# Performance work log

Measured on AMD Instinct MI355X. Metric: run time of the kernel, lower is better.

The kernel has to match this reference:

```python
import jax, jax.numpy as jnp
import numpy as np

INPUT_DIM = 1024
HIDDEN_DIM = 1024


def setup_inputs() -> dict:
    key = jax.random.key(0)
    k1, k2, k3, k4, k5 = jax.random.split(key, 5)
    B, T = 64, 512
    bound_h = 1.0 / np.sqrt(HIDDEN_DIM)
    bound_x = 1.0 / np.sqrt(INPUT_DIM)
    return {
        "x_seq": jax.random.normal(k1, (B, T, INPUT_DIM), dtype=jnp.float32),
        "W_h": jax.random.uniform(k2, (HIDDEN_DIM, HIDDEN_DIM), jnp.float32, -bound_h, bound_h),
        "b_h": jax.random.uniform(k3, (HIDDEN_DIM,), jnp.float32, -bound_h, bound_h),
        "W_x": jax.random.uniform(k4, (HIDDEN_DIM, INPUT_DIM), jnp.float32, -bound_x, bound_x),
        "b_x": jax.random.uniform(k5, (HIDDEN_DIM,), jnp.float32, -bound_x, bound_x),
    }


def reference(x_seq, W_h, b_h, W_x, b_x):
    # Precompute input projection for all timesteps as one batched GEMM:
    # xp: [B, T, H]
    xp = jnp.einsum("bti,hi->bth", x_seq, W_x) + b_x
    B = x_seq.shape[0]
    h0 = jnp.zeros((B, HIDDEN_DIM), dtype=x_seq.dtype)

    def step(h, xp_t):
        # h: [B, H], xp_t: [B, H]
        h_new = jnp.tanh(h @ W_h.T + b_h + xp_t)
        return h_new, None

    # scan over time: xp transposed to [T, B, H]
    h_final, _ = jax.lax.scan(step, h0, jnp.swapaxes(xp, 0, 1))
    return h_final  # [B, H] — last hidden state per batch element
```

## Files before the change

kernel.cpp:

```cpp
#include <hip/hip_runtime.h>
#include <cmath>


#define Bsz 64
#define Tsz 512
#define Hsz 1024

typedef float  f32x4 __attribute__((ext_vector_type(4)));
typedef short  s16x8 __attribute__((ext_vector_type(8)));

#define AS1 __attribute__((address_space(1)))
#define AS3 __attribute__((address_space(3)))

__device__ __forceinline__ unsigned short f2bf(float f) {
  unsigned u = __float_as_uint(f);
  u += 0x7fff + ((u >> 16) & 1);
  return (unsigned short)(u >> 16);
}

__device__ __forceinline__ void pack8(unsigned short* d, float4 v0, float4 v1) {
  d[0] = f2bf(v0.x); d[1] = f2bf(v0.y); d[2] = f2bf(v0.z); d[3] = f2bf(v0.w);
  d[4] = f2bf(v1.x); d[5] = f2bf(v1.y); d[6] = f2bf(v1.z); d[7] = f2bf(v1.w);
}

__device__ __forceinline__ float fast_tanh(float x) {
  float e = __expf(2.0f * x);
  return 1.0f - 2.0f / (e + 1.0f);
}

__global__ __launch_bounds__(256) void cvt_kernel(
    const float* __restrict__ x, const float* __restrict__ Wx,
    unsigned short* __restrict__ xb, unsigned short* __restrict__ wxb) {
  const long long NX = (long long)Bsz * Tsz * Hsz / 8;
  const long long NW = (long long)Hsz * Hsz / 8;
  const long long stride = (long long)gridDim.x * 256;
  for (long long i = (long long)blockIdx.x * 256 + threadIdx.x;
       i < NX + NW; i += stride) {
    const float* s; unsigned short* d; long long j;
    if (i < NX) { s = x;  d = xb;  j = i; }
    else        { s = Wx; d = wxb; j = i - NX; }
    const float4 a = *(const float4*)(s + j * 8);
    const float4 b = *(const float4*)(s + j * 8 + 4);
    unsigned short tmp[8];
    pack8(tmp, a, b);
    *(s16x8*)(d + j * 8) = *(const s16x8*)tmp;
  }
}

__global__ __launch_bounds__(256) void xp_gemm128_kernel(
    const unsigned short* __restrict__ xb, const unsigned short* __restrict__ wxb,
    const float* __restrict__ bx, const float* __restrict__ bh,
    float* __restrict__ xp) {
  __shared__ __align__(16) unsigned short Al[128 * 32];
  __shared__ __align__(16) unsigned short Bl[128 * 32];

  const int tid  = threadIdx.x;
  const int w    = tid >> 6;
  const int lane = tid & 63;
  const int m    = lane & 15;
  const int q    = lane >> 4;
  const int wy   = w >> 1;
  const int wx   = w & 1;
  const int row0 = blockIdx.x * 128;
  const int col0 = blockIdx.y * 128;

  f32x4 acc[4][4];
#pragma unroll
  for (int i = 0; i < 4; ++i)
#pragma unroll
    for (int j = 0; j < 4; ++j) acc[i][j] = (f32x4){0.f, 0.f, 0.f, 0.f};

  const int lrow = lane >> 2;
  const int lch  = lane & 3;

  for (int kt = 0; kt < 32; ++kt) {
    const int kb = kt * 32;
#pragma unroll
    for (int i = 0; i < 2; ++i) {
      const int ra  = w * 32 + i * 16 + lrow;
      const int scs = lch ^ ((ra >> 1) & 3);
      const unsigned short* gA = xb  + (size_t)(row0 + ra) * 1024 + kb + scs * 8;
      const unsigned short* gB = wxb + (size_t)(col0 + ra) * 1024 + kb + scs * 8;
      __builtin_amdgcn_global_load_lds(
          (const AS1 void*)gA, (AS3 void*)&Al[(w * 32 + i * 16) * 32], 16, 0, 0);
      __builtin_amdgcn_global_load_lds(
          (const AS1 void*)gB, (AS3 void*)&Bl[(w * 32 + i * 16) * 32], 16, 0, 0);
    }
    __syncthreads();

    s16x8 af[4], bf[4];
#pragma unroll
    for (int mt = 0; mt < 4; ++mt) {
      const int ar = wy * 64 + mt * 16 + m;
      af[mt] = *(const s16x8*)&Al[ar * 32 + ((q ^ ((ar >> 1) & 3)) << 3)];
    }
#pragma unroll
    for (int nt = 0; nt < 4; ++nt) {
      const int br = wx * 64 + nt * 16 + m;
      bf[nt] = *(const s16x8*)&Bl[br * 32 + ((q ^ ((br >> 1) & 3)) << 3)];
    }
#pragma unroll
    for (int mt = 0; mt < 4; ++mt)
#pragma unroll
      for (int nt = 0; nt < 4; ++nt)
        acc[mt][nt] = __builtin_amdgcn_mfma_f32_16x16x32_bf16(
            af[mt], bf[nt], acc[mt][nt], 0, 0, 0);
    __syncthreads();
  }

#pragma unroll
  for (int nt = 0; nt < 4; ++nt) {
    const int col  = col0 + wx * 64 + nt * 16 + m;
    const float bias = bx[col] + bh[col];
#pragma unroll
    for (int mt = 0; mt < 4; ++mt) {
#pragma unroll
      for (int r = 0; r < 4; ++r) {
        const int rowg = row0 + wy * 64 + mt * 16 + q * 4 + r;
        const int b = rowg >> 9;
        const int t = rowg & 511;
        xp[(size_t)t * (Bsz * Hsz) + b * Hsz + col] = acc[mt][nt][r] + bias;
      }
    }
  }
}

__global__ __launch_bounds__(256) void xp_gemm_f32_kernel(
    const float* __restrict__ x, const float* __restrict__ Wx,
    const float* __restrict__ bx, const float* __restrict__ bh,
    float* __restrict__ xp) {
  __shared__ unsigned short Al[64 * 32];
  __shared__ unsigned short Bl[64 * 32];

  const int tid  = threadIdx.x;
  const int w    = tid >> 6;
  const int lane = tid & 63;
  const int m    = lane & 15;
  const int q    = lane >> 4;
  const int row0 = blockIdx.x * 64;
  const int col0 = blockIdx.y * 64;

  f32x4 acc[4];
#pragma unroll
  for (int i = 0; i < 4; ++i) acc[i] = (f32x4){0.f, 0.f, 0.f, 0.f};

  const int sr = tid >> 2;
  const int sc = tid & 3;
  const int sw = sc ^ ((sr >> 1) & 3);

  for (int kt = 0; kt < 32; ++kt) {
    const int k0 = kt * 32 + sc * 8;
    {
      const float* p = x + (size_t)(row0 + sr) * 1024 + k0;
      pack8(&Al[sr * 32 + sw * 8], *(const float4*)p, *(const float4*)(p + 4));
    }
    {
      const float* p = Wx + (size_t)(col0 + sr) * 1024 + k0;
      pack8(&Bl[sr * 32 + sw * 8], *(const float4*)p, *(const float4*)(p + 4));
    }
    __syncthreads();
    const int arow = w * 16 + m;
    s16x8 a = *(const s16x8*)&Al[arow * 32 + ((q ^ ((arow >> 1) & 3)) << 3)];
#pragma unroll
    for (int nt = 0; nt < 4; ++nt) {
      const int nrow = nt * 16 + m;
      s16x8 b = *(const s16x8*)&Bl[nrow * 32 + ((q ^ ((nrow >> 1) & 3)) << 3)];
      acc[nt] = __builtin_amdgcn_mfma_f32_16x16x32_bf16(a, b, acc[nt], 0, 0, 0);
    }
    __syncthreads();
  }

#pragma unroll
  for (int nt = 0; nt < 4; ++nt) {
    const int col  = col0 + nt * 16 + m;
    const float bias = bx[col] + bh[col];
#pragma unroll
    for (int r = 0; r < 4; ++r) {
      const int rowg = row0 + w * 16 + q * 4 + r;
      const int b = rowg >> 9;
      const int t = rowg & 511;
      xp[(size_t)t * (Bsz * Hsz) + b * Hsz + col] = acc[nt][r] + bias;
    }
  }
}


__global__ __launch_bounds__(64, 1) void rnn_scan_kernel(
    const float* __restrict__ Wh, const float* __restrict__ xp,
    float* __restrict__ out,
    unsigned long long* __restrict__ ring, unsigned* __restrict__ flags) {
  __shared__ unsigned short Wl[16 * 1024];

  const int lane = threadIdx.x & 63;
  const int m    = lane & 15;
  const int q    = lane >> 4;
  const int gb   = blockIdx.x >> 6;
  const int gj   = blockIdx.x & 63;
  const int j0   = gj * 16;
  const int rb   = gb * 16;

  for (int i = 0; i < 32; ++i) {
    const int jr = i >> 1;
    const int c  = (i & 1) * 64 + lane;
    const float* p = Wh + (size_t)(j0 + jr) * 1024 + c * 8;
    pack8(&Wl[jr * 1024 + ((c ^ (jr & 7)) << 3)],
          *(const float4*)p, *(const float4*)(p + 4));
  }
  __syncthreads();

  unsigned* grpflags = flags + gb * 1024;
  unsigned* myflag   = grpflags + gj * 16;
  const unsigned* pollflag = grpflags + lane * 16;

  unsigned long long* const grp = ring + (size_t)gb * 4096;
  const int cons_off = q * 32 + m * 2;
  const int prod_off = (gj * 2 + (q >> 1)) * 32 + m * 2 + (q & 1);

  for (int t = 0; t < Tsz; ++t) {
    const float4 xv = *(const float4*)(
        xp + (size_t)t * (Bsz * Hsz) + (size_t)(rb + m) * Hsz + j0 + q * 4);
    const float* xf = (const float*)&xv;

    f32x4 acc0 = (f32x4){0.f, 0.f, 0.f, 0.f};
    f32x4 acc1 = (f32x4){0.f, 0.f, 0.f, 0.f};
    f32x4 acc2 = (f32x4){0.f, 0.f, 0.f, 0.f};
    f32x4 acc3 = (f32x4){0.f, 0.f, 0.f, 0.f};

    if (t > 0) {
      const unsigned tg = (unsigned)t;
      unsigned v = __hip_atomic_load(pollflag, __ATOMIC_RELAXED,
                                     __HIP_MEMORY_SCOPE_AGENT);
      while (!__all((int)(v >= tg))) {
        __builtin_amdgcn_s_sleep(1);
        v = __hip_atomic_load(pollflag, __ATOMIC_RELAXED,
                              __HIP_MEMORY_SCOPE_AGENT);
      }

      const unsigned long long* rbase =
          grp + (size_t)(t & 1) * 16384 + cons_off;
      unsigned long long d[64];
#pragma unroll
      for (int kk = 0; kk < 32; ++kk) {
        d[2 * kk]     = __hip_atomic_load(rbase + kk * 128,     __ATOMIC_RELAXED,
                                          __HIP_MEMORY_SCOPE_AGENT);
        d[2 * kk + 1] = __hip_atomic_load(rbase + kk * 128 + 1, __ATOMIC_RELAXED,
                                          __HIP_MEMORY_SCOPE_AGENT);
      }

#pragma unroll
      for (int kk = 0; kk < 32; ++kk) {
        union { unsigned long long u[2]; s16x8 v; } hb;
        hb.u[0] = d[2 * kk];
        hb.u[1] = d[2 * kk + 1];
        s16x8 wf = *(const s16x8*)&Wl[m * 1024 + (((kk * 4 + q) ^ (m & 7)) << 3)];
        f32x4& ac = ((kk & 3) == 0) ? acc0 : ((kk & 3) == 1) ? acc1
                   : ((kk & 3) == 2) ? acc2 : acc3;
        ac = __builtin_amdgcn_mfma_f32_16x16x32_bf16(wf, hb.v, ac, 0, 0, 0);
      }
    }

    const f32x4 accs = (acc0 + acc1) + (acc2 + acc3);
    float hv[4];
#pragma unroll
    for (int r = 0; r < 4; ++r) hv[r] = fast_tanh(accs[r] + xf[r]);

    if (t == Tsz - 1) {
      *(float4*)&out[(size_t)(rb + m) * Hsz + j0 + q * 4] =
          make_float4(hv[0], hv[1], hv[2], hv[3]);
    } else {
      const unsigned long long s =
          (unsigned long long)f2bf(hv[0])        |
          ((unsigned long long)f2bf(hv[1]) << 16) |
          ((unsigned long long)f2bf(hv[2]) << 32) |
          ((unsigned long long)f2bf(hv[3]) << 48);
      unsigned long long* wb =
          grp + (size_t)((t + 1) & 1) * 16384 + prod_off;
      __hip_atomic_store(wb, s, __ATOMIC_RELAXED, __HIP_MEMORY_SCOPE_AGENT);
      asm volatile("s_waitcnt vmcnt(0)" ::: "memory");
      if (lane == 0)
        __hip_atomic_store(myflag, (unsigned)(t + 1), __ATOMIC_RELAXED,
                           __HIP_MEMORY_SCOPE_AGENT);
    }
  }
}

extern "C" void kernel_launch(void* const* d_in, const int* in_sizes, int n_in,
                              void* d_out, int out_size, void* d_ws, size_t ws_size,
                              hipStream_t stream) {
  (void)in_sizes; (void)n_in; (void)out_size;
  const float* x  = (const float*)d_in[0];
  const float* Wh = (const float*)d_in[1];
  const float* bh = (const float*)d_in[2];
  const float* Wx = (const float*)d_in[3];
  const float* bx = (const float*)d_in[4];
  float* out = (float*)d_out;

  char* ws = (char*)d_ws;
  unsigned*           flags = (unsigned*)ws;
  unsigned long long* ring  = (unsigned long long*)(ws + 65536);
  const size_t off_xp  = (size_t)1 << 20;
  const size_t off_xb  = off_xp + (size_t)Bsz * Tsz * Hsz * 4;
  const size_t off_wxb = off_xb + (size_t)Bsz * Tsz * Hsz * 2;
  const size_t need    = off_wxb + (size_t)Hsz * Hsz * 2;
  float*          xp  = (float*)(ws + off_xp);
  unsigned short* xb  = (unsigned short*)(ws + off_xb);
  unsigned short* wxb = (unsigned short*)(ws + off_wxb);

  hipMemsetAsync(d_ws, 0, 16384, stream);

  if (ws_size >= need) {
    cvt_kernel<<<dim3(2048), dim3(256), 0, stream>>>(x, Wx, xb, wxb);
    xp_gemm128_kernel<<<dim3(256, 8), dim3(256), 0, stream>>>(xb, wxb, bx, bh, xp);
  } else {
    dim3 g1(Bsz * Tsz / 64, Hsz / 64);
    xp_gemm_f32_kernel<<<g1, dim3(256), 0, stream>>>(x, Wx, bx, bh, xp);
  }
  rnn_scan_kernel<<<dim3(256), dim3(64), 0, stream>>>(Wh, xp, out, ring, flags);
}
```

Baseline: 1.642 ms.

## Double-buffer xp GEMM LDS tiles with K=64 stages

Restructures the input-projection GEMM to use two LDS buffers and a K-step of 64. The next tile's global_load_lds is issued before the MFMAs on the current tile, so loads can overlap compute, and the syncthreads per K-step drop from two to one. The XOR swizzle is reworked for the wider 64-element rows. This quadruples LDS use per block, which may reduce occupancy. The GEMM is only part of total time, since the recurrent scan likely dominates.

New measurement: 1.631 ms. Within noise of the previous version (-0.7%).

```diff
diff --git a/kernel.cpp b/kernel.cpp
--- a/kernel.cpp
+++ b/kernel.cpp
@@ -51,8 +51,8 @@
     const unsigned short* __restrict__ xb, const unsigned short* __restrict__ wxb,
     const float* __restrict__ bx, const float* __restrict__ bh,
     float* __restrict__ xp) {
-  __shared__ __align__(16) unsigned short Al[128 * 32];
-  __shared__ __align__(16) unsigned short Bl[128 * 32];
+  __shared__ __align__(16) unsigned short Al[2][128 * 64];
+  __shared__ __align__(16) unsigned short Bl[2][128 * 64];
 
   const int tid  = threadIdx.x;
   const int w    = tid >> 6;
@@ -70,43 +70,62 @@
 #pragma unroll
     for (int j = 0; j < 4; ++j) acc[i][j] = (f32x4){0.f, 0.f, 0.f, 0.f};
 
-  const int lrow = lane >> 2;
-  const int lch  = lane & 3;
-
-  for (int kt = 0; kt < 32; ++kt) {
-    const int kb = kt * 32;
-#pragma unroll
-    for (int i = 0; i < 2; ++i) {
-      const int ra  = w * 32 + i * 16 + lrow;
-      const int scs = lch ^ ((ra >> 1) & 3);
-      const unsigned short* gA = xb  + (size_t)(row0 + ra) * 1024 + kb + scs * 8;
-      const unsigned short* gB = wxb + (size_t)(col0 + ra) * 1024 + kb + scs * 8;
-      __builtin_amdgcn_global_load_lds(
-          (const AS1 void*)gA, (AS3 void*)&Al[(w * 32 + i * 16) * 32], 16, 0, 0);
-      __builtin_amdgcn_global_load_lds(
-          (const AS1 void*)gB, (AS3 void*)&Bl[(w * 32 + i * 16) * 32], 16, 0, 0);
-    }
+  const int scs = (lane & 7) ^ (lane >> 3);
+  const unsigned short* pA[4];
+  const unsigned short* pB[4];
+#pragma unroll
+  for (int i = 0; i < 4; ++i) {
+    const int ra = w * 32 + i * 8 + (lane >> 3);
+    pA[i] = xb  + (size_t)(row0 + ra) * 1024 + scs * 8;
+    pB[i] = wxb + (size_t)(col0 + ra) * 1024 + scs * 8;
+  }
+
+#define STAGE(BUF)                                                            \
+  do {                                                                        \
+    _Pragma("unroll")                                                         \
+    for (int i_ = 0; i_ < 4; ++i_) {                                          \
+      __builtin_amdgcn_global_load_lds((const AS1 void*)pA[i_],               \
+          (AS3 void*)&Al[BUF][(w * 32 + i_ * 8) * 64], 16, 0, 0);             \
+      __builtin_amdgcn_global_load_lds((const AS1 void*)pB[i_],               \
+          (AS3 void*)&Bl[BUF][(w * 32 + i_ * 8) * 64], 16, 0, 0);             \
+      pA[i_] += 64; pB[i_] += 64;                                             \
+    }                                                                         \
+  } while (0)
+
+  STAGE(0);
+  __syncthreads();
+
+  int cur = 0;
+  for (int kt = 0; kt < 16; ++kt) {
+    if (kt < 15) STAGE(cur ^ 1);
+
+#pragma unroll
+    for (int kk2 = 0; kk2 < 2; ++kk2) {
+      s16x8 af[4], bf4[4];
+#pragma unroll
+      for (int mt = 0; mt < 4; ++mt) {
+        const int ar = wy * 64 + mt * 16 + m;
+        af[mt] = *(const s16x8*)
+            &Al[cur][ar * 64 + (((kk2 * 4 + q) ^ (m & 7)) << 3)];
+      }
+#pragma unroll
+      for (int nt = 0; nt < 4; ++nt) {
+        const int br = wx * 64 + nt * 16 + m;
+        bf4[nt] = *(const s16x8*)
+            &Bl[cur][br * 64 + (((kk2 * 4 + q) ^ (m & 7)) << 3)];
+      }
+#pragma unroll
+      for (int mt = 0; mt < 4; ++mt)
+#pragma unroll
+        for (int nt = 0; nt < 4; ++nt)
+          acc[mt][nt] = __builtin_amdgcn_mfma_f32_16x16x32_bf16(
+              af[mt], bf4[nt], acc[mt][nt], 0, 0, 0);
+    }
+
     __syncthreads();
-
-    s16x8 af[4], bf[4];
-#pragma unroll
-    for (int mt = 0; mt < 4; ++mt) {
-      const int ar = wy * 64 + mt * 16 + m;
-      af[mt] = *(const s16x8*)&Al[ar * 32 + ((q ^ ((ar >> 1) & 3)) << 3)];
-    }
-#pragma unroll
-    for (int nt = 0; nt < 4; ++nt) {
-      const int br = wx * 64 + nt * 16 + m;
-      bf[nt] = *(const s16x8*)&Bl[br * 32 + ((q ^ ((br >> 1) & 3)) << 3)];
-    }
-#pragma unroll
-    for (int mt = 0; mt < 4; ++mt)
-#pragma unroll
-      for (int nt = 0; nt < 4; ++nt)
-        acc[mt][nt] = __builtin_amdgcn_mfma_f32_16x16x32_bf16(
-            af[mt], bf[nt], acc[mt][nt], 0, 0, 0);
-    __syncthreads();
-  }
+    cur ^= 1;
+  }
+#undef STAGE
 
 #pragma unroll
   for (int nt = 0; nt < 4; ++nt) {
```
